# Kernel tuning notes

Measured on AMD Instinct MI355X. Metric: run time of the kernel, lower is better.

## Reference

```python
import jax, jax.numpy as jnp
import numpy as np

B, H, E, G, SEQ_LEN = 131072, 64, 16, 32, 30


def setup_inputs() -> dict:
    key = jax.random.key(0)
    ks = jax.random.split(key, 17)
    def lin(kw, kb, out_f, in_f):
        s = 1.0 / np.sqrt(in_f)
        W = jax.random.uniform(kw, (out_f, in_f), jnp.float32, -s, s)
        b = jax.random.uniform(kb, (out_f,), jnp.float32, -s, s)
        return W, b
    W_se, b_se = lin(ks[0], ks[1], E, 2)
    W_h2p, b_h2p = lin(ks[2], ks[3], 2, 3 * H)
    W_goal, b_goal = lin(ks[4], ks[5], H, 2 * G)
    W_abs, b_abs = lin(ks[6], ks[7], H, 2)
    W_ih, b_ih = lin(ks[8], ks[9], 4 * H, E)
    W_hh, b_hh = lin(ks[10], ks[11], 4 * H, H)
    return {
        "traj_abs": jax.random.normal(ks[12], (1, B, 2), jnp.float32),
        "traj_rel": jax.random.normal(ks[13], (1, B, 2), jnp.float32),
        "h0": jax.random.normal(ks[14], (1, B, H), jnp.float32),
        "c0": jax.random.normal(ks[15], (1, B, H), jnp.float32),
        "goals": jax.random.normal(ks[16], (B, G, 2), jnp.float32),
        "W_ih": W_ih, "W_hh": W_hh, "b_ih": b_ih, "b_hh": b_hh,
        "W_se": W_se, "b_se": b_se,
        "W_h2p": W_h2p, "b_h2p": b_h2p,
        "W_goal": W_goal, "b_goal": b_goal,
        "W_abs": W_abs, "b_abs": b_abs,
    }


def reference(traj_abs, traj_rel, h0, c0, goals,
              W_ih, W_hh, b_ih, b_hh,
              W_se, b_se, W_h2p, b_h2p,
              W_goal, b_goal, W_abs, b_abs):
    b = traj_abs.shape[1]
    goal_emb = goals.reshape(b, -1) @ W_goal.T + b_goal            # (b, H)
    dec_in = jax.nn.leaky_relu(traj_rel[0] @ W_se.T + b_se)        # (b, E)

    def step(carry, _):
        h, c, x, abs_pos = carry
        gates = x @ W_ih.T + b_ih + h @ W_hh.T + b_hh              # (b, 4H)
        i, f, g, o = jnp.split(gates, 4, axis=-1)                  # PyTorch gate order
        c = jax.nn.sigmoid(f) * c + jax.nn.sigmoid(i) * jnp.tanh(g)
        h = jax.nn.sigmoid(o) * jnp.tanh(c)
        abs_emb = abs_pos @ W_abs.T + b_abs                        # (b, H)
        inp = jnp.concatenate([h, abs_emb, goal_emb], axis=1)      # (b, 3H)
        rel = inp @ W_h2p.T + b_h2p                                # (b, 2)
        x = jax.nn.leaky_relu(rel @ W_se.T + b_se)
        return (h, c, x, abs_pos + rel), rel

    _, rels = jax.lax.scan(step, (h0[0], c0[0], dec_in, traj_abs[0]),
                           None, length=SEQ_LEN)
    return rels  # (seq_len, b, 2)
```

## Files before the change

kernel.cpp:

```cpp
#include <hip/hip_runtime.h>
#include <stdint.h>


#define B_TOT 131072
#define SEQL 30

typedef _Float16 f16x8 __attribute__((ext_vector_type(8)));
typedef _Float16 f16x2 __attribute__((ext_vector_type(2)));
typedef float f32x4 __attribute__((ext_vector_type(4)));

__device__ __forceinline__ float fexp2(float x) {
#if __has_builtin(__builtin_amdgcn_exp2f)
  return __builtin_amdgcn_exp2f(x);
#else
  return exp2f(x);
#endif
}
__device__ __forceinline__ float frcp(float x) {
#if __has_builtin(__builtin_amdgcn_rcpf)
  return __builtin_amdgcn_rcpf(x);
#else
  return 1.0f / x;
#endif
}

__global__ void setup_consts(const float* __restrict__ Wgoal,
                             const float* __restrict__ bgoal,
                             const float* __restrict__ Wh2p,
                             const float* __restrict__ bh2p,
                             const float* __restrict__ Wabs,
                             const float* __restrict__ babs,
                             float* __restrict__ wsf) {
  const int tid = threadIdx.x;
  const int wv = tid >> 6;
  const int lane = tid & 63;
  if (wv == 0) {
    const int k = lane;
    float s0 = 0.f, s1 = 0.f;
#pragma unroll 8
    for (int jj = 0; jj < 64; ++jj) {
      float wg = Wgoal[jj * 64 + k];
      s0 += wg * Wh2p[128 + jj];
      s1 += wg * Wh2p[320 + jj];
    }
    wsf[k] = s0;
    wsf[64 + k] = s1;
  } else {
    const int i = lane >> 3, sub = lane & 7;
    const int p = i & 1, grp = i >> 1;
    float s = 0.f;
#pragma unroll
    for (int t = 0; t < 8; ++t) {
      int j = sub * 8 + t;
      float wv_ = (grp < 3) ? Wh2p[p * 192 + 64 + j] : Wh2p[p * 192 + 128 + j];
      float av = (grp == 0)   ? Wabs[j * 2 + 0]
                 : (grp == 1) ? Wabs[j * 2 + 1]
                 : (grp == 2) ? babs[j]
                              : bgoal[j];
      s += av * wv_;
    }
    s += __shfl_xor(s, 1, 64);
    s += __shfl_xor(s, 2, 64);
    s += __shfl_xor(s, 4, 64);
    if (sub == 0) {
      if (grp == 2) s += bh2p[p];
      wsf[128 + i] = s;
    }
  }
}

__global__ __launch_bounds__(256, 3) void lstm_mfma(
    const float* __restrict__ tabs, const float* __restrict__ trel,
    const float* __restrict__ h0, const float* __restrict__ c0,
    const float* __restrict__ goals, const float* __restrict__ Wih,
    const float* __restrict__ Whh, const float* __restrict__ bih,
    const float* __restrict__ bhh, const float* __restrict__ Wse,
    const float* __restrict__ bse, const float* __restrict__ Wh2p,
    const float* __restrict__ wsf, float* __restrict__ outp) {
  const int lane = threadIdx.x & 63;
  const int w = threadIdx.x >> 6;
  const int q = lane >> 4;
  const int n = lane & 15;
  const int hs = 16 * w;
  const int bbase = blockIdx.x * 16;

  __shared__ __align__(16) _Float16 hbuf[2 * 16 * 72];

  const float SI = -1.4426950408889634f;
  const float SG = 2.8853900817779268f;
  const float gsc[4] = {SI, SI, SG, SI};
  f16x8 bw[4][3];
#pragma unroll
  for (int g = 0; g < 4; ++g) {
    const int row = g * 64 + hs + n;
    const float sc = gsc[g];
#pragma unroll
    for (int kk = 0; kk < 2; ++kk)
#pragma unroll
      for (int j = 0; j < 8; ++j)
        bw[g][kk][j] = (_Float16)(sc * Whh[row * 64 + kk * 32 + q * 8 + j]);
    float bias = sc * (bih[row] + bhh[row]);
#pragma unroll
    for (int j = 0; j < 8; ++j) {
      float v = (q < 2) ? sc * Wih[row * 16 + q * 8 + j]
                        : ((q == 2 && j == 0) ? bias : 0.f);
      bw[g][2][j] = (_Float16)v;
    }
  }
  f16x8 awp0, awp1;
#pragma unroll
  for (int j = 0; j < 8; ++j) {
    float v0 = (n < 2) ? Wh2p[n * 192 + q * 8 + j] : 0.f;
    float v1 = (n < 2) ? Wh2p[n * 192 + 32 + q * 8 + j] : 0.f;
    awp0[j] = (_Float16)v0;
    awp1[j] = (_Float16)v1;
  }
  const float Sx0 = wsf[128], Sx1 = wsf[129];
  const float Sy0 = wsf[130], Sy1 = wsf[131];

  f16x2 wsaP[4], wsbP[4], bscP[4];
#pragma unroll
  for (int jj = 0; jj < 4; ++jj) {
    if (q < 2) {
      int kx = q * 8 + 2 * jj;
      wsaP[jj] = f16x2{(_Float16)Wse[kx * 2 + 0], (_Float16)Wse[kx * 2 + 2]};
      wsbP[jj] = f16x2{(_Float16)Wse[kx * 2 + 1], (_Float16)Wse[kx * 2 + 3]};
      bscP[jj] = f16x2{(_Float16)bse[kx], (_Float16)bse[kx + 1]};
    } else {
      wsaP[jj] = f16x2{(_Float16)0.f, (_Float16)0.f};
      wsbP[jj] = wsaP[jj];
      bscP[jj] = (jj == 0 && q == 2) ? f16x2{(_Float16)1.f, (_Float16)0.f}
                                     : wsaP[jj];
    }
  }
  const f16x2 cA = f16x2{(_Float16)0.505f, (_Float16)0.505f};
  const f16x2 cB = f16x2{(_Float16)0.495f, (_Float16)0.495f};

  auto build_x = [&](float r0f, float r1f) -> f16x8 {
    f16x2 r0h = f16x2{(_Float16)r0f, (_Float16)r0f};
    f16x2 r1h = f16x2{(_Float16)r1f, (_Float16)r1f};
    f16x8 xr;
#pragma unroll
    for (int jj = 0; jj < 4; ++jj) {
      f16x2 t = r0h * wsaP[jj] + (r1h * wsbP[jj] + bscP[jj]);
      uint32_t tu = __builtin_bit_cast(uint32_t, t);
      f16x2 ta = __builtin_bit_cast(f16x2, tu & 0x7FFF7FFFu);
      f16x2 lr = cA * t + cB * ta;
      xr[2 * jj] = lr[0];
      xr[2 * jj + 1] = lr[1];
    }
    return xr;
  };

  const f32x4 zC = {0.f, 0.f, 0.f, 0.f};
  f32x4 GaccT;
  {
    f16x8 aM0, aM1, bg0, bg1;
#pragma unroll
    for (int j = 0; j < 8; ++j) {
      int k = q * 8 + j;
      aM0[j] = (_Float16)((n < 2) ? wsf[n * 64 + k] : 0.f);
      aM1[j] = (_Float16)((n < 2) ? wsf[n * 64 + 32 + k] : 0.f);
      bg0[j] = (_Float16)goals[(bbase + n) * 64 + k];
      bg1[j] = (_Float16)goals[(bbase + n) * 64 + 32 + k];
    }
    GaccT = __builtin_amdgcn_mfma_f32_16x16x32_f16(aM0, bg0, zC, 0, 0, 0);
    GaccT = __builtin_amdgcn_mfma_f32_16x16x32_f16(aM1, bg1, GaccT, 0, 0, 0);
    GaccT[0] += wsf[132] + wsf[134];
    GaccT[1] += wsf[133] + wsf[135];
  }

  float ax = tabs[(bbase + n) * 2 + 0];
  float ay = tabs[(bbase + n) * 2 + 1];
  float cst[4];
#pragma unroll
  for (int r = 0; r < 4; ++r) {
    const int b = bbase + 4 * q + r;
    cst[r] = c0[b * 64 + hs + n];
    hbuf[(4 * q + r) * 72 + hs + n] = (_Float16)h0[b * 64 + hs + n];
  }

  f16x8 xf = build_x(trel[(bbase + n) * 2 + 0], trel[(bbase + n) * 2 + 1]);

  const int ro = n * 72 + q * 8;
  const int wo = (4 * q) * 72 + hs + n;
  const float K2 = 2.8853900817779268f;

  int poff = 0;
  for (int s = 0; s <= SEQL; ++s) {
    __syncthreads();
    const f16x8 ah0 = *(const f16x8*)(hbuf + poff + ro);
    const f16x8 ah1 = *(const f16x8*)(hbuf + poff + ro + 32);

    if (s > 0) {
      f32x4 pa =
          __builtin_amdgcn_mfma_f32_16x16x32_f16(awp0, ah0, GaccT, 0, 0, 0);
      pa = __builtin_amdgcn_mfma_f32_16x16x32_f16(awp1, ah1, pa, 0, 0, 0);
      float u0 = pa[0] + fmaf(ax, Sx0, ay * Sy0);
      float u1 = pa[1] + fmaf(ax, Sx1, ay * Sy1);
      ax += u0;
      ay += u1;
      if (w == 0 && lane < 16) {
        float2 v;
        v.x = u0;
        v.y = u1;
        ((float2*)outp)[(size_t)(s - 1) * B_TOT + bbase + lane] = v;
      }
      float r0b = __shfl(u0, n, 64);
      float r1b = __shfl(u1, n, 64);
      xf = build_x(r0b, r1b);
    }

    if (s < SEQL) {
      f32x4 acc[4];
#pragma unroll
      for (int g = 0; g < 4; ++g) {
        f32x4 a = __builtin_amdgcn_mfma_f32_16x16x32_f16(ah0, bw[g][0], zC,
                                                         0, 0, 0);
        a = __builtin_amdgcn_mfma_f32_16x16x32_f16(ah1, bw[g][1], a, 0, 0, 0);
        a = __builtin_amdgcn_mfma_f32_16x16x32_f16(xf, bw[g][2], a, 0, 0, 0);
        acc[g] = a;
      }
      _Float16* hw = hbuf + (poff ^ 1152) + wo;
#pragma unroll
      for (int r = 0; r < 4; ++r) {
        float A = fexp2(acc[0][r]);
        float Fv = fexp2(acc[1][r]);
        float Bv = fexp2(acc[2][r]);
        float t1 = 1.f + A;
        float t2 = Bv + 1.f;
        float t3 = 1.f + Fv;
        float t4 = Bv - 1.f;
        float m1 = t1 * t2;
        float num = fmaf(cst[r], m1, t4 * t3);
        float c = num * frcp(m1 * t3);
        cst[r] = c;
        float Cv = fexp2(acc[3][r]);
        float Dv = fexp2(K2 * c);
        float hn = (Dv - 1.f) * frcp((1.f + Cv) * (Dv + 1.f));
        hw[72 * r] = (_Float16)hn;
      }
      poff ^= 1152;
    }
  }
}

extern "C" void kernel_launch(void* const* d_in, const int* in_sizes, int n_in,
                              void* d_out, int out_size, void* d_ws,
                              size_t ws_size, hipStream_t stream) {
  (void)in_sizes; (void)n_in; (void)out_size; (void)ws_size;
  const float* tabs  = (const float*)d_in[0];
  const float* trel  = (const float*)d_in[1];
  const float* h0    = (const float*)d_in[2];
  const float* c0    = (const float*)d_in[3];
  const float* goals = (const float*)d_in[4];
  const float* Wih   = (const float*)d_in[5];
  const float* Whh   = (const float*)d_in[6];
  const float* bih   = (const float*)d_in[7];
  const float* bhh   = (const float*)d_in[8];
  const float* Wse   = (const float*)d_in[9];
  const float* bse   = (const float*)d_in[10];
  const float* Wh2p  = (const float*)d_in[11];
  const float* bh2p  = (const float*)d_in[12];
  const float* Wgoal = (const float*)d_in[13];
  const float* bgoal = (const float*)d_in[14];
  const float* Wabs  = (const float*)d_in[15];
  const float* babs  = (const float*)d_in[16];
  float* wsf = (float*)d_ws;

  setup_consts<<<dim3(1), dim3(128), 0, stream>>>(Wgoal, bgoal, Wh2p, bh2p,
                                                  Wabs, babs, wsf);
  lstm_mfma<<<dim3(8192), dim3(256), 0, stream>>>(
      tabs, trel, h0, c0, goals, Wih, Whh, bih, bhh, Wse, bse, Wh2p, wsf,
      (float*)d_out);
}
```

Measured before the change: 532.3 us.

## Fold leaky-ReLU linear part into LSTM input weights and pack gate math

Rewrites leaky_relu(t) as 0.505*t + 0.495*|t|. The linear 0.505 part is folded into the W_ih MFMA B-operand through extra bias and rel-coefficient slots, so build_x only computes the scaled |t| term plus raw rel values. The h2p A-matrix rows are replicated so every lane gets u0/u1 directly, which removes the two cross-lane shuffles per step. The gate nonlinearity math is regrouped into float2 vectors so the compiler can emit packed FP32 ops. The folded weights are stored in fp16, which changes rounding slightly.

```diff
diff --git a/kernel.cpp b/kernel.cpp
--- a/kernel.cpp
+++ b/kernel.cpp
@@ -8,6 +8,7 @@
 typedef _Float16 f16x8 __attribute__((ext_vector_type(8)));
 typedef _Float16 f16x2 __attribute__((ext_vector_type(2)));
 typedef float f32x4 __attribute__((ext_vector_type(4)));
+typedef float f32x2 __attribute__((ext_vector_type(2)));
 
 __device__ __forceinline__ float fexp2(float x) {
 #if __has_builtin(__builtin_amdgcn_exp2f)
@@ -81,6 +82,7 @@
   const int w = threadIdx.x >> 6;
   const int q = lane >> 4;
   const int n = lane & 15;
+  const int pm = n & 3;
   const int hs = 16 * w;
   const int bbase = blockIdx.x * 16;
 
@@ -99,19 +101,36 @@
 #pragma unroll
       for (int j = 0; j < 8; ++j)
         bw[g][kk][j] = (_Float16)(sc * Whh[row * 64 + kk * 32 + q * 8 + j]);
-    float bias = sc * (bih[row] + bhh[row]);
+    float bfold = 0.f, m20 = 0.f, m21 = 0.f;
+#pragma unroll
+    for (int k = 0; k < 16; ++k) {
+      float wik = Wih[row * 16 + k];
+      bfold += bse[k] * wik;
+      m20 += Wse[k * 2 + 0] * wik;
+      m21 += Wse[k * 2 + 1] * wik;
+    }
+    float bias = sc * (bih[row] + bhh[row] + 0.505f * bfold);
 #pragma unroll
     for (int j = 0; j < 8; ++j) {
-      float v = (q < 2) ? sc * Wih[row * 16 + q * 8 + j]
-                        : ((q == 2 && j == 0) ? bias : 0.f);
+      float v;
+      if (q < 2)
+        v = sc * Wih[row * 16 + q * 8 + j];
+      else if (q == 2 && j == 0)
+        v = bias;
+      else if (q == 2 && j == 1)
+        v = sc * 0.505f * m20;
+      else if (q == 2 && j == 2)
+        v = sc * 0.505f * m21;
+      else
+        v = 0.f;
       bw[g][2][j] = (_Float16)v;
     }
   }
   f16x8 awp0, awp1;
 #pragma unroll
   for (int j = 0; j < 8; ++j) {
-    float v0 = (n < 2) ? Wh2p[n * 192 + q * 8 + j] : 0.f;
-    float v1 = (n < 2) ? Wh2p[n * 192 + 32 + q * 8 + j] : 0.f;
+    float v0 = (pm < 2) ? Wh2p[pm * 192 + q * 8 + j] : 0.f;
+    float v1 = (pm < 2) ? Wh2p[pm * 192 + 32 + q * 8 + j] : 0.f;
     awp0[j] = (_Float16)v0;
     awp1[j] = (_Float16)v1;
   }
@@ -119,22 +138,34 @@
   const float Sy0 = wsf[130], Sy1 = wsf[131];
 
   f16x2 wsaP[4], wsbP[4], bscP[4];
+  const uint32_t xmask = (q < 2) ? 0x7FFF7FFFu : 0xFFFFFFFFu;
 #pragma unroll
   for (int jj = 0; jj < 4; ++jj) {
+    f16x2 z = f16x2{(_Float16)0.f, (_Float16)0.f};
     if (q < 2) {
       int kx = q * 8 + 2 * jj;
-      wsaP[jj] = f16x2{(_Float16)Wse[kx * 2 + 0], (_Float16)Wse[kx * 2 + 2]};
-      wsbP[jj] = f16x2{(_Float16)Wse[kx * 2 + 1], (_Float16)Wse[kx * 2 + 3]};
-      bscP[jj] = f16x2{(_Float16)bse[kx], (_Float16)bse[kx + 1]};
+      wsaP[jj] =
+          f16x2{(_Float16)(0.495f * Wse[kx * 2 + 0]),
+                (_Float16)(0.495f * Wse[kx * 2 + 2])};
+      wsbP[jj] =
+          f16x2{(_Float16)(0.495f * Wse[kx * 2 + 1]),
+                (_Float16)(0.495f * Wse[kx * 2 + 3])};
+      bscP[jj] = f16x2{(_Float16)(0.495f * bse[kx]),
+                       (_Float16)(0.495f * bse[kx + 1])};
+    } else if (q == 2 && jj == 0) {
+      wsaP[jj] = f16x2{(_Float16)0.f, (_Float16)1.f};
+      wsbP[jj] = z;
+      bscP[jj] = f16x2{(_Float16)1.f, (_Float16)0.f};
+    } else if (q == 2 && jj == 1) {
+      wsaP[jj] = z;
+      wsbP[jj] = f16x2{(_Float16)1.f, (_Float16)0.f};
+      bscP[jj] = z;
     } else {
-      wsaP[jj] = f16x2{(_Float16)0.f, (_Float16)0.f};
-      wsbP[jj] = wsaP[jj];
-      bscP[jj] = (jj == 0 && q == 2) ? f16x2{(_Float16)1.f, (_Float16)0.f}
-                                     : wsaP[jj];
-    }
-  }
-  const f16x2 cA = f16x2{(_Float16)0.505f, (_Float16)0.505f};
-  const f16x2 cB = f16x2{(_Float16)0.495f, (_Float16)0.495f};
+      wsaP[jj] = z;
+      wsbP[jj] = z;
+      bscP[jj] = z;
+    }
+  }
 
   auto build_x = [&](float r0f, float r1f) -> f16x8 {
     f16x2 r0h = f16x2{(_Float16)r0f, (_Float16)r0f};
@@ -143,9 +174,8 @@
 #pragma unroll
     for (int jj = 0; jj < 4; ++jj) {
       f16x2 t = r0h * wsaP[jj] + (r1h * wsbP[jj] + bscP[jj]);
-      uint32_t tu = __builtin_bit_cast(uint32_t, t);
-      f16x2 ta = __builtin_bit_cast(f16x2, tu & 0x7FFF7FFFu);
-      f16x2 lr = cA * t + cB * ta;
+      uint32_t tu = __builtin_bit_cast(uint32_t, t) & xmask;
+      f16x2 lr = __builtin_bit_cast(f16x2, tu);
       xr[2 * jj] = lr[0];
       xr[2 * jj + 1] = lr[1];
     }
@@ -159,8 +189,8 @@
 #pragma unroll
     for (int j = 0; j < 8; ++j) {
       int k = q * 8 + j;
-      aM0[j] = (_Float16)((n < 2) ? wsf[n * 64 + k] : 0.f);
-      aM1[j] = (_Float16)((n < 2) ? wsf[n * 64 + 32 + k] : 0.f);
+      aM0[j] = (_Float16)((pm < 2) ? wsf[pm * 64 + k] : 0.f);
+      aM1[j] = (_Float16)((pm < 2) ? wsf[pm * 64 + 32 + k] : 0.f);
       bg0[j] = (_Float16)goals[(bbase + n) * 64 + k];
       bg1[j] = (_Float16)goals[(bbase + n) * 64 + 32 + k];
     }
@@ -206,9 +236,7 @@
         v.y = u1;
         ((float2*)outp)[(size_t)(s - 1) * B_TOT + bbase + lane] = v;
       }
-      float r0b = __shfl(u0, n, 64);
-      float r1b = __shfl(u1, n, 64);
-      xf = build_x(r0b, r1b);
+      xf = build_x(u0, u1);
     }
 
     if (s < SEQL) {
@@ -223,22 +251,30 @@
       }
       _Float16* hw = hbuf + (poff ^ 1152) + wo;
 #pragma unroll
-      for (int r = 0; r < 4; ++r) {
-        float A = fexp2(acc[0][r]);
-        float Fv = fexp2(acc[1][r]);
-        float Bv = fexp2(acc[2][r]);
-        float t1 = 1.f + A;
-        float t2 = Bv + 1.f;
-        float t3 = 1.f + Fv;
-        float t4 = Bv - 1.f;
-        float m1 = t1 * t2;
-        float num = fmaf(cst[r], m1, t4 * t3);
-        float c = num * frcp(m1 * t3);
-        cst[r] = c;
-        float Cv = fexp2(acc[3][r]);
-        float Dv = fexp2(K2 * c);
-        float hn = (Dv - 1.f) * frcp((1.f + Cv) * (Dv + 1.f));
-        hw[72 * r] = (_Float16)hn;
+      for (int pr = 0; pr < 2; ++pr) {
+        const int ra = 2 * pr, rb = 2 * pr + 1;
+        f32x2 Av = {fexp2(acc[0][ra]), fexp2(acc[0][rb])};
+        f32x2 Fv = {fexp2(acc[1][ra]), fexp2(acc[1][rb])};
+        f32x2 Bv = {fexp2(acc[2][ra]), fexp2(acc[2][rb])};
+        const f32x2 one = {1.f, 1.f};
+        f32x2 t1 = Av + one;
+        f32x2 t2 = Bv + one;
+        f32x2 t3 = Fv + one;
+        f32x2 t4 = Bv - one;
+        f32x2 m1 = t1 * t2;
+        f32x2 cs = {cst[ra], cst[rb]};
+        f32x2 num = cs * m1 + t4 * t3;
+        f32x2 den = m1 * t3;
+        f32x2 cc = {num[0] * frcp(den[0]), num[1] * frcp(den[1])};
+        cst[ra] = cc[0];
+        cst[rb] = cc[1];
+        f32x2 Cv = {fexp2(acc[3][ra]), fexp2(acc[3][rb])};
+        f32x2 k2c = cc * K2;
+        f32x2 Dv = {fexp2(k2c[0]), fexp2(k2c[1])};
+        f32x2 hd = (Cv + one) * (Dv + one);
+        f32x2 hnm = Dv - one;
+        hw[72 * ra] = (_Float16)(hnm[0] * frcp(hd[0]));
+        hw[72 * rb] = (_Float16)(hnm[1] * frcp(hd[1]));
       }
       poff ^= 1152;
     }
```

After: 539.5 us. No clear change (+1.4%).
